# Optimization experiments

Hardware: AMD Instinct MI355X
Metric: run time of the kernel (lower is better)

## Reference

```python
import jax, jax.numpy as jnp
from jax import lax
import numpy as np


def setup_inputs() -> dict:
    key = jax.random.key(0)
    ks = jax.random.split(key, 9)
    B, T, H = 64, 4096, 128
    G = 4 * H
    s = 1.0 / np.sqrt(H)  # PyTorch LSTM default init scale
    return {
        "data": jax.random.normal(ks[0], (B, T, 1), dtype=jnp.float32),
        "h0": jax.random.normal(ks[1], (B, H), dtype=jnp.float32),
        "c0": jax.random.normal(ks[2], (B, H), dtype=jnp.float32),
        "W_ih": jax.random.uniform(ks[3], (G, 1), jnp.float32, -s, s),
        "W_hh": jax.random.uniform(ks[4], (G, H), jnp.float32, -s, s),
        "b_ih": jax.random.uniform(ks[5], (G,), jnp.float32, -s, s),
        "b_hh": jax.random.uniform(ks[6], (G,), jnp.float32, -s, s),
        "W_out": jax.random.uniform(ks[7], (1, H), jnp.float32, -s, s),
        "b_out": jax.random.uniform(ks[8], (1,), jnp.float32, -s, s),
    }


def reference(data, h0, c0, W_ih, W_hh, b_ih, b_hh, W_out, b_out):
    # Single-layer batch-first LSTM (PyTorch gate order i,f,g,o), then Linear on last step.
    H = h0.shape[-1]
    # Precompute input projections for all timesteps: [B, T, 4H] -> time-major [T, B, 4H]
    x_proj = jnp.einsum("bti,gi->btg", data, W_ih) + b_ih + b_hh
    x_proj = jnp.swapaxes(x_proj, 0, 1)

    def step(carry, xg):
        h, c = carry
        gates = xg + h @ W_hh.T  # [B, 4H]
        i = jax.nn.sigmoid(gates[:, 0 * H:1 * H])
        f = jax.nn.sigmoid(gates[:, 1 * H:2 * H])
        g = jnp.tanh(gates[:, 2 * H:3 * H])
        o = jax.nn.sigmoid(gates[:, 3 * H:4 * H])
        c = f * c + i * g
        h = o * jnp.tanh(c)
        return (h, c), None

    (hT, _), _ = lax.scan(step, (h0, c0), x_proj)
    # out[:, -1, :] of the LSTM is hT; final linear projection -> [B, 1]
    return hT @ W_out.T + b_out
```

## Files before the change

kernel.cpp:

```cpp
#include <hip/hip_runtime.h>
#include <math.h>

constexpr int Hdim = 128;
constexpr int TMAX = 4096;

typedef _Float16 v8h __attribute__((ext_vector_type(8)));
typedef float v4f __attribute__((ext_vector_type(4)));

template <int CTRL>
__device__ __forceinline__ float dppf(float v) {
  return __int_as_float(
      __builtin_amdgcn_update_dpp(0, __float_as_int(v), CTRL, 0xF, 0xF, true));
}

#if __has_builtin(__builtin_amdgcn_exp2f)
__device__ __forceinline__ float exp2_fast(float x) {
  return __builtin_amdgcn_exp2f(x);
}
#else
__device__ __forceinline__ float exp2_fast(float x) {
  return __expf(x * 0.6931471805599453f);
}
#endif

__device__ __forceinline__ float sel4(v4f d, int r) {
  const float s01 = (r & 1) ? d.y : d.x;
  const float s23 = (r & 1) ? d.w : d.z;
  return (r & 2) ? s23 : s01;
}

__global__ __launch_bounds__(512) void lstm_mfma(
    const float* __restrict__ data, const float* __restrict__ h0,
    const float* __restrict__ c0, const float* __restrict__ W_ih,
    const float* __restrict__ W_hh, const float* __restrict__ b_ih,
    const float* __restrict__ b_hh, const float* __restrict__ W_out,
    const float* __restrict__ b_out, float* __restrict__ out, int T) {
  __shared__ __align__(16) float xs[TMAX];
  __shared__ __align__(16) _Float16 hbuf[2][Hdim];

  const int b = blockIdx.x;
  const int tid = threadIdx.x;
  const int lane = tid & 63;
  const int wv = tid >> 6;
  const int p = lane >> 4;
  const int m = lane & 15;
  const int q = m & 3;
  const int s = m >> 2;
  const int el = 16 * wv + 4 * p + s;

  {
    const float4* src = (const float4*)(data + (size_t)b * T);
    float4* dst = (float4*)xs;
    for (int i = tid; i < T / 4; i += 512) dst[i] = src[i];
  }

  constexpr float L2E = 1.44269504088896f;

  v8h a[4][4];
#pragma unroll
  for (int g = 0; g < 4; ++g) {
    const int row = 128 * g + 16 * wv + m;
    const float Mr = (g == 2) ? 2.0f * L2E : -L2E;
    const float* wr = W_hh + (size_t)row * Hdim + 8 * p;
#pragma unroll
    for (int c = 0; c < 4; ++c) {
      float4 v0 = ((const float4*)(wr + 32 * c))[0];
      float4 v1 = ((const float4*)(wr + 32 * c))[1];
      a[g][c] = v8h{(_Float16)(Mr * v0.x), (_Float16)(Mr * v0.y),
                    (_Float16)(Mr * v0.z), (_Float16)(Mr * v0.w),
                    (_Float16)(Mr * v1.x), (_Float16)(Mr * v1.y),
                    (_Float16)(Mr * v1.z), (_Float16)(Mr * v1.w)};
    }
  }

  v4f acc_init[4];
#pragma unroll
  for (int g = 0; g < 4; ++g) {
    const float Mr = (g == 2) ? 2.0f * L2E : -L2E;
    const int row = 128 * g + 16 * wv + 4 * p;
    acc_init[g] = v4f{Mr * (b_ih[row + 0] + b_hh[row + 0]),
                      Mr * (b_ih[row + 1] + b_hh[row + 1]),
                      Mr * (b_ih[row + 2] + b_hh[row + 2]),
                      Mr * (b_ih[row + 3] + b_hh[row + 3])};
  }

  const float MkL = (q == 2) ? 2.0f * L2E : -L2E;
  const float wihL = MkL * W_ih[128 * q + el];
  const float As = (q == 2) ? -2.0f : 1.0f;
  const float Bs = (q == 2) ? 1.0f : 0.0f;

  float cst = c0[(size_t)b * Hdim + el];
  if (tid < 128) hbuf[0][tid] = (_Float16)h0[(size_t)b * Hdim + tid];
  __syncthreads();

  for (int t0 = 0; t0 < T; t0 += 4) {
    const float4 xv = *(const float4*)&xs[t0];
    const float xts[4] = {xv.x, xv.y, xv.z, xv.w};
#pragma unroll
    for (int u = 0; u < 4; ++u) {
      const int t = t0 + u;
      const _Float16* hb = hbuf[t & 1];
      v8h bq[4];
#pragma unroll
      for (int c = 0; c < 4; ++c) bq[c] = *(const v8h*)(hb + 32 * c + 8 * p);
      const float xt = xts[u];

      v4f d0 = acc_init[0], d1 = acc_init[1], d2 = acc_init[2],
          d3 = acc_init[3];
#pragma unroll
      for (int c = 0; c < 4; ++c) {
        d0 = __builtin_amdgcn_mfma_f32_16x16x32_f16(a[0][c], bq[c], d0, 0, 0, 0);
        d1 = __builtin_amdgcn_mfma_f32_16x16x32_f16(a[1][c], bq[c], d1, 0, 0, 0);
        d2 = __builtin_amdgcn_mfma_f32_16x16x32_f16(a[2][c], bq[c], d2, 0, 0, 0);
        d3 = __builtin_amdgcn_mfma_f32_16x16x32_f16(a[3][c], bq[c], d3, 0, 0, 0);
      }

      const float z0 = sel4(d0, s);
      const float z1 = sel4(d1, s);
      const float z2 = sel4(d2, s);
      const float z3 = sel4(d3, s);
      const float zq = (q & 2) ? ((q & 1) ? z3 : z2) : ((q & 1) ? z1 : z0);

      const float y =
          fmaf(As, __builtin_amdgcn_rcpf(1.0f + exp2_fast(fmaf(xt, wihL, zq))),
               Bs);

      const float yi = dppf<0x00>(y);
      const float yf = dppf<0x55>(y);
      const float yg = dppf<0xAA>(y);
      const float yo = dppf<0xFF>(y);

      cst = fmaf(yf, cst, yi * yg);
      const float th = fmaf(
          -2.0f, __builtin_amdgcn_rcpf(1.0f + exp2_fast(cst * (2.0f * L2E))),
          1.0f);
      const float h = yo * th;

      if (q == 0) hbuf[(t + 1) & 1][el] = (_Float16)h;
      __syncthreads();
    }
  }

  if (tid < 64) {
    const _Float16* hf = hbuf[T & 1];
    float sum =
        (float)hf[tid] * W_out[tid] + (float)hf[tid + 64] * W_out[tid + 64];
#pragma unroll
    for (int off = 32; off > 0; off >>= 1) sum += __shfl_down(sum, off, 64);
    if (tid == 0) out[b] = sum + b_out[0];
  }
}

extern "C" void kernel_launch(void* const* d_in, const int* in_sizes, int n_in,
                              void* d_out, int out_size, void* d_ws,
                              size_t ws_size, hipStream_t stream) {
  const float* data = (const float*)d_in[0];
  const float* h0 = (const float*)d_in[1];
  const float* c0 = (const float*)d_in[2];
  const float* W_ih = (const float*)d_in[3];
  const float* W_hh = (const float*)d_in[4];
  const float* b_ih = (const float*)d_in[5];
  const float* b_hh = (const float*)d_in[6];
  const float* W_out = (const float*)d_in[7];
  const float* b_out = (const float*)d_in[8];
  float* out = (float*)d_out;

  const int B = in_sizes[1] / Hdim;
  const int T = in_sizes[0] / B;

  lstm_mfma<<<B, 512, 0, stream>>>(data, h0, c0, W_ih, W_hh, b_ih, b_hh,
                                   W_out, b_out, out, T);
}
```

Baseline: 1.747 ms.

## Split hidden-dim reduction between MFMA and per-lane fdot2 for last 32 columns

Cuts the MFMA chain per gate from four K-chunks to three and computes the remaining 32 columns of each lane's own gate row with packed fp16 dot2 instructions on the vector ALU. The aim is to shorten the serial MFMA dependency latency in every recurrent step by letting VALU work run alongside the matrix unit. In exchange each lane holds 16 extra packed weight registers and does four broadcast LDS reads plus 16 dot2 operations per step, and the fdot2 path accumulates serially in one register.

Result: slower. 2.066 ms (+18.3%).

```diff
diff --git a/kernel.cpp b/kernel.cpp
--- a/kernel.cpp
+++ b/kernel.cpp
@@ -5,6 +5,7 @@
 constexpr int TMAX = 4096;
 
 typedef _Float16 v8h __attribute__((ext_vector_type(8)));
+typedef _Float16 v2h __attribute__((ext_vector_type(2)));
 typedef float v4f __attribute__((ext_vector_type(4)));
 
 template <int CTRL>
@@ -56,14 +57,14 @@
 
   constexpr float L2E = 1.44269504088896f;
 
-  v8h a[4][4];
+  v8h a[4][3];
 #pragma unroll
   for (int g = 0; g < 4; ++g) {
     const int row = 128 * g + 16 * wv + m;
     const float Mr = (g == 2) ? 2.0f * L2E : -L2E;
     const float* wr = W_hh + (size_t)row * Hdim + 8 * p;
 #pragma unroll
-    for (int c = 0; c < 4; ++c) {
+    for (int c = 0; c < 3; ++c) {
       float4 v0 = ((const float4*)(wr + 32 * c))[0];
       float4 v1 = ((const float4*)(wr + 32 * c))[1];
       a[g][c] = v8h{(_Float16)(Mr * v0.x), (_Float16)(Mr * v0.y),
@@ -73,6 +74,16 @@
     }
   }
 
+  const int rowt = 128 * q + el;
+  const float Mt = (q == 2) ? 2.0f * L2E : -L2E;
+  v2h wt[16];
+  {
+    const float* wrt = W_hh + (size_t)rowt * Hdim + 96;
+#pragma unroll
+    for (int j = 0; j < 16; ++j)
+      wt[j] = v2h{(_Float16)(Mt * wrt[2 * j]), (_Float16)(Mt * wrt[2 * j + 1])};
+  }
+
   v4f acc_init[4];
 #pragma unroll
   for (int g = 0; g < 4; ++g) {
@@ -84,8 +95,7 @@
                       Mr * (b_ih[row + 3] + b_hh[row + 3])};
   }
 
-  const float MkL = (q == 2) ? 2.0f * L2E : -L2E;
-  const float wihL = MkL * W_ih[128 * q + el];
+  const float wihL = Mt * W_ih[rowt];
   const float As = (q == 2) ? -2.0f : 1.0f;
   const float Bs = (q == 2) ? 1.0f : 0.0f;
 
@@ -100,30 +110,52 @@
     for (int u = 0; u < 4; ++u) {
       const int t = t0 + u;
       const _Float16* hb = hbuf[t & 1];
-      v8h bq[4];
-#pragma unroll
-      for (int c = 0; c < 4; ++c) bq[c] = *(const v8h*)(hb + 32 * c + 8 * p);
+      v8h bq[3];
+#pragma unroll
+      for (int c = 0; c < 3; ++c) bq[c] = *(const v8h*)(hb + 32 * c + 8 * p);
+      const v8h ht0 = *(const v8h*)(hb + 96);
+      const v8h ht1 = *(const v8h*)(hb + 104);
+      const v8h ht2 = *(const v8h*)(hb + 112);
+      const v8h ht3 = *(const v8h*)(hb + 120);
       const float xt = xts[u];
 
       v4f d0 = acc_init[0], d1 = acc_init[1], d2 = acc_init[2],
           d3 = acc_init[3];
 #pragma unroll
-      for (int c = 0; c < 4; ++c) {
+      for (int c = 0; c < 3; ++c) {
         d0 = __builtin_amdgcn_mfma_f32_16x16x32_f16(a[0][c], bq[c], d0, 0, 0, 0);
         d1 = __builtin_amdgcn_mfma_f32_16x16x32_f16(a[1][c], bq[c], d1, 0, 0, 0);
         d2 = __builtin_amdgcn_mfma_f32_16x16x32_f16(a[2][c], bq[c], d2, 0, 0, 0);
         d3 = __builtin_amdgcn_mfma_f32_16x16x32_f16(a[3][c], bq[c], d3, 0, 0, 0);
       }
 
+      float zt = 0.f;
+#pragma unroll
+      for (int j = 0; j < 4; ++j)
+        zt = __builtin_amdgcn_fdot2(
+            wt[j], v2h{ht0[2 * j], ht0[2 * j + 1]}, zt, false);
+#pragma unroll
+      for (int j = 0; j < 4; ++j)
+        zt = __builtin_amdgcn_fdot2(
+            wt[4 + j], v2h{ht1[2 * j], ht1[2 * j + 1]}, zt, false);
+#pragma unroll
+      for (int j = 0; j < 4; ++j)
+        zt = __builtin_amdgcn_fdot2(
+            wt[8 + j], v2h{ht2[2 * j], ht2[2 * j + 1]}, zt, false);
+#pragma unroll
+      for (int j = 0; j < 4; ++j)
+        zt = __builtin_amdgcn_fdot2(
+            wt[12 + j], v2h{ht3[2 * j], ht3[2 * j + 1]}, zt, false);
+
       const float z0 = sel4(d0, s);
       const float z1 = sel4(d1, s);
       const float z2 = sel4(d2, s);
       const float z3 = sel4(d3, s);
       const float zq = (q & 2) ? ((q & 1) ? z3 : z2) : ((q & 1) ? z1 : z0);
 
-      const float y =
-          fmaf(As, __builtin_amdgcn_rcpf(1.0f + exp2_fast(fmaf(xt, wihL, zq))),
-               Bs);
+      const float y = fmaf(
+          As, __builtin_amdgcn_rcpf(1.0f + exp2_fast(fmaf(xt, wihL, zq + zt))),
+          Bs);
 
       const float yi = dppf<0x00>(y);
       const float yf = dppf<0x55>(y);
```
